# Kernel optimization log

Measured on AMD Instinct MI355X. Metric: run time of the kernel, lower is better.

The kernel has to match this reference:

```python
import jax, jax.numpy as jnp
import numpy as np
from jax import lax

B, N, NB = 1, 1600, 200
NOTE, ENC, ENCVEC = 128, 64, 16
OUT, MARGIN, TREG = 11, 32, 32
E = 12
FIN = NOTE + ENC + 2 * TREG + OUT + MARGIN   # 299 = net_params.final.input
SEC = OUT + MARGIN                           # 43 = GatedGraph secondary size
FBH = NOTE + ENC                             # final_beat_hidden_idx
SEQ_IT, G_IT = 2, 3
HEADS_M = 8


def setup_inputs():
    key = jax.random.key(0)
    ks = iter(jax.random.split(key, 64))
    nrm = lambda shape, s=0.05: jax.random.normal(next(ks), shape, jnp.float32) * s
    zeros = lambda shape: jnp.zeros(shape, jnp.float32)
    inp = {}
    inp["note_out"] = jax.random.normal(next(ks), (B, N, NOTE), jnp.float32)
    inp["perf_vec"] = jax.random.normal(next(ks), (B, ENCVEC), jnp.float32)
    inp["res_info"] = jax.random.normal(next(ks), (B, NB, 8), jnp.float32)
    # sparse musical-graph adjacency, one matrix per edge type
    inp["edges"] = (jax.random.uniform(next(ks), (E, N, N)) < 0.004).astype(jnp.float32)
    # sorted beat index per note, every beat non-empty (8 notes per beat)
    inp["beat_numbers"] = jnp.arange(N, dtype=jnp.int32) // (N // NB)
    inp["w_style"] = nrm((ENCVEC, ENC)); inp["b_style"] = zeros((ENC,))
    inp["w_init1"] = nrm((NOTE, ENC)); inp["b_init1"] = zeros((ENC,))
    inp["w_init2"] = nrm((ENC, OUT)); inp["b_init2"] = zeros((OUT,))
    inp["gg_wa"] = nrm((E, FIN, FIN)); inp["gg_ba"] = zeros((FIN,))
    inp["gg_wz"] = nrm((FIN, SEC)); inp["gg_wr"] = nrm((FIN, SEC)); inp["gg_wh"] = nrm((FIN, SEC))
    inp["gg_uz"] = nrm((SEC, SEC)); inp["gg_ur"] = nrm((SEC, SEC)); inp["gg_uh"] = nrm((SEC, SEC))
    inp["att_beat_w"] = nrm((OUT, OUT)); inp["att_beat_b"] = zeros((OUT,)); inp["att_beat_c"] = nrm((1, OUT), 1.0)
    inp["att_marg_w"] = nrm((MARGIN, MARGIN)); inp["att_marg_b"] = zeros((MARGIN,))
    inp["att_marg_c"] = nrm((HEADS_M, MARGIN // HEADS_M), 1.0)
    rnn_in = MARGIN + OUT + 8
    for l, din in ((0, rnn_in), (1, 2 * TREG)):
        for d in "fb":
            inp[f"lstm_wih_{l}{d}"] = nrm((4 * TREG, din))
            inp[f"lstm_whh_{l}{d}"] = nrm((4 * TREG, TREG))
            inp[f"lstm_b_{l}{d}"] = zeros((4 * TREG,))
    inp["w_tempo"] = nrm((2 * TREG, 1)); inp["b_tempo"] = zeros((1,))
    inp["w_fc1"] = nrm((FIN, MARGIN)); inp["b_fc1"] = zeros((MARGIN,))
    inp["w_fc2"] = nrm((MARGIN, OUT - 1)); inp["b_fc2"] = zeros((OUT - 1,))
    return inp


def _gated_graph(h, edges, wa, ba, wz, wr, wh, uz, ur, uh, iters):
    # h: (B,N,FIN), edges: (E,N,N). GGNN update on last SEC features.
    for _ in range(iters):
        agg = jnp.einsum('eij,bid->ebjd', edges, h)          # incoming msgs per edge type
        act = jnp.einsum('ebjd,eds->bjs', agg, wa) + ba      # (B,N,FIN)
        hs = h[..., -SEC:]
        z = jax.nn.sigmoid(act @ wz + hs @ uz)
        r = jax.nn.sigmoid(act @ wr + hs @ ur)
        cand = jnp.tanh(act @ wh + (r * hs) @ uh)
        hs = (1.0 - z) * hs + z * cand
        h = jnp.concatenate([h[..., :-SEC], hs], -1)
    return h


def _seg_attention(x, W, b, ctx, seg, num_seg):
    # ContextAttention pooled per beat segment (make_higher_node).
    Bb, T, D = x.shape
    H, hd = ctx.shape
    a = jnp.tanh(x @ W + b).reshape(Bb, T, H, hd)
    sim = jnp.einsum('bthd,hd->bth', a, ctx)
    def smax(s):  # segment softmax over notes within each beat, (T,H)
        m = jax.ops.segment_max(s, seg, num_segments=num_seg)
        e = jnp.exp(s - m[seg])
        zz = jax.ops.segment_sum(e, seg, num_segments=num_seg)
        return e / zz[seg]
    w = jax.vmap(smax)(sim)                                   # (B,T,H)
    xh = x.reshape(Bb, T, H, hd)
    pool = jax.vmap(lambda wi, xi: jax.ops.segment_sum(wi[:, :, None] * xi, seg, num_segments=num_seg))(w, xh)
    return pool.reshape(Bb, num_seg, D)


def _lstm_dir(x, wih, whh, b, reverse):
    Bb = x.shape[0]; H = whh.shape[1]
    def step(carry, xt):
        h, c = carry
        g = xt @ wih.T + h @ whh.T + b
        i, f, gg, o = jnp.split(g, 4, -1)
        c = jax.nn.sigmoid(f) * c + jax.nn.sigmoid(i) * jnp.tanh(gg)
        h = jax.nn.sigmoid(o) * jnp.tanh(c)
        return (h, c), h
    init = (jnp.zeros((Bb, H), x.dtype), jnp.zeros((Bb, H), x.dtype))
    _, hs = lax.scan(step, init, jnp.swapaxes(x, 0, 1), reverse=reverse)
    return jnp.swapaxes(hs, 0, 1)


def _bilstm(x, layers):
    for (wf, uf, bf, wb, ub, bb) in layers:
        x = jnp.concatenate([_lstm_dir(x, wf, uf, bf, False), _lstm_dir(x, wb, ub, bb, True)], -1)
    return x


def _forward(note_out, perf_vec, res_info, edges, beat_numbers,
             w_style, b_style, w_init1, b_init1, w_init2, b_init2,
             gg_wa, gg_ba, gg_wz, gg_wr, gg_wh, gg_uz, gg_ur, gg_uh,
             att_beat_w, att_beat_b, att_beat_c, att_marg_w, att_marg_b, att_marg_c,
             lstm_wih_0f, lstm_whh_0f, lstm_b_0f, lstm_wih_0b, lstm_whh_0b, lstm_b_0b,
             lstm_wih_1f, lstm_whh_1f, lstm_b_1f, lstm_wih_1b, lstm_whh_1b, lstm_b_1b,
             w_tempo, b_tempo, w_fc1, b_fc1, w_fc2, b_fc2):
    Bb, Nn, _ = note_out.shape
    # style_vector_expandor (dropout = identity in eval), broadcast to notes
    perf_z = jax.nn.relu(perf_vec @ w_style + b_style)
    perf_z = jnp.broadcast_to(perf_z[:, None, :], (Bb, Nn, ENC))
    init_out = jax.nn.relu(note_out @ w_init1 + b_init1) @ w_init2 + b_init2
    beat_hid0 = jnp.zeros((Bb, Nn, 2 * TREG), note_out.dtype)
    margin0 = jnp.zeros((Bb, Nn, MARGIN), note_out.dtype)
    out = jnp.concatenate([note_out, perf_z, beat_hid0, init_out, margin0], -1)  # (B,N,FIN)
    lstm_layers = [(lstm_wih_0f, lstm_whh_0f, lstm_b_0f, lstm_wih_0b, lstm_whh_0b, lstm_b_0b),
                   (lstm_wih_1f, lstm_whh_1f, lstm_b_1f, lstm_wih_1b, lstm_whh_1b, lstm_b_1b)]
    total = [init_out]
    final_out = init_out
    for _ in range(SEQ_IT):
        out = _gated_graph(out, edges, gg_wa, gg_ba, gg_wz, gg_wr, gg_wh, gg_uz, gg_ur, gg_uh, G_IT)
        init_o = out[..., -SEC:-MARGIN]          # (B,N,OUT)
        marg = out[..., -MARGIN:]                # (B,N,MARGIN)
        marg_beat = _seg_attention(marg, att_marg_w, att_marg_b, att_marg_c, beat_numbers, NB)
        out_beat = _seg_attention(init_o, att_beat_w, att_beat_b, att_beat_c, beat_numbers, NB)
        beat_cat = jnp.concatenate([out_beat, marg_beat, res_info], -1)  # (B,NB,51)
        rnn = _bilstm(beat_cat, lstm_layers)                             # (B,NB,64)
        tempo = rnn @ w_tempo + b_tempo                                  # (B,NB,1)
        tempos_sp = tempo[:, beat_numbers, :]    # span_beat_to_note_num
        rnn_sp = rnn[:, beat_numbers, :]
        out = jnp.concatenate([out[..., :FBH], rnn_sp, out[..., -SEC:]], -1)
        other = jax.nn.relu(out @ w_fc1 + b_fc1) @ w_fc2 + b_fc2         # (B,N,OUT-1)
        final_out = jnp.concatenate([tempos_sp, other], -1)              # (B,N,OUT)
        out = jnp.concatenate([out[..., :-SEC], final_out, out[..., -MARGIN:]], -1)
        total.append(final_out)
    return final_out, jnp.stack(total, 0)


def reference(note_out, perf_vec, res_info, edges, beat_numbers,
              w_style, b_style, w_init1, b_init1, w_init2, b_init2,
              gg_wa, gg_ba, gg_wz, gg_wr, gg_wh, gg_uz, gg_ur, gg_uh,
              att_beat_w, att_beat_b, att_beat_c, att_marg_w, att_marg_b, att_marg_c,
              lstm_wih_0f, lstm_whh_0f, lstm_b_0f, lstm_wih_0b, lstm_whh_0b, lstm_b_0b,
              lstm_wih_1f, lstm_whh_1f, lstm_b_1f, lstm_wih_1b, lstm_whh_1b, lstm_b_1b,
              w_tempo, b_tempo, w_fc1, b_fc1, w_fc2, b_fc2):
    return _forward(note_out, perf_vec, res_info, edges, beat_numbers,
                    w_style, b_style, w_init1, b_init1, w_init2, b_init2,
                    gg_wa, gg_ba, gg_wz, gg_wr, gg_wh, gg_uz, gg_ur, gg_uh,
                    att_beat_w, att_beat_b, att_beat_c, att_marg_w, att_marg_b, att_marg_c,
                    lstm_wih_0f, lstm_whh_0f, lstm_b_0f, lstm_wih_0b, lstm_whh_0b, lstm_b_0b,
                    lstm_wih_1f, lstm_whh_1f, lstm_b_1f, lstm_wih_1b, lstm_whh_1b, lstm_b_1b,
                    w_tempo, b_tempo, w_fc1, b_fc1, w_fc2, b_fc2)
```

## Files before the change

### kernel.cpp

```cpp
#include <hip/hip_runtime.h>
#include <stdint.h>

#define NN     1600
#define NBEAT  200
#define FINW   299
#define HSTR   300
#define SECW   43
#define EDG    12
#define C3     129
#define CM     128
#define DEG_CAP 256

#define NB_WA3   450
#define NB_INIT8 200
#define NB_SCAN  2560

#define K1C (-1.4426950408889634f)
#define K2C (-2.8853900817779268f)

#if __has_builtin(__builtin_amdgcn_exp2f)
__device__ __forceinline__ float fexp2(float x){ return __builtin_amdgcn_exp2f(x); }
#else
__device__ __forceinline__ float fexp2(float x){ return exp2f(x); }
#endif
#if __has_builtin(__builtin_amdgcn_rcpf)
__device__ __forceinline__ float frcp(float x){ return __builtin_amdgcn_rcpf(x); }
#else
__device__ __forceinline__ float frcp(float x){ return 1.0f/x; }
#endif

__device__ __forceinline__ float sigm(float x){ return frcp(1.f + fexp2(K1C*x)); }
__device__ __forceinline__ float tanh_(float x){ return __builtin_fmaf(frcp(1.f + fexp2(K2C*x)), 2.f, -1.f); }

__device__ __forceinline__ float gate_scale(int col){
  return (col >= 64 && col < 96) ? K2C : K1C;
}

__device__ __forceinline__ float swap_lo_to_hi(float v){
#if __has_builtin(__builtin_amdgcn_permlane32_swap)
  typedef unsigned u32x2 __attribute__((ext_vector_type(2)));
  u32x2 r = __builtin_amdgcn_permlane32_swap(__float_as_uint(v), __float_as_uint(v), false, false);
  return __uint_as_float(r[0]);
#else
  return __shfl(v, (int)(threadIdx.x & 31), 64);
#endif
}

constexpr size_t OFF_H    = 0;
constexpr size_t OFF_WA3  = OFF_H    + (size_t)NN*HSTR;
constexpr size_t OFF_WA3X = OFF_WA3  + (size_t)EDG*FINW*CM;
constexpr size_t OFF_B3   = OFF_WA3X + (size_t)EDG*FINW;
constexpr size_t OFF_MST  = OFF_B3   + 132;
constexpr size_t OFF_MSTX = OFF_MST  + (size_t)EDG*NN*CM;
constexpr size_t OFF_M3   = OFF_MSTX + (size_t)EDG*NN;
constexpr size_t OFF_M3X  = OFF_M3   + (size_t)EDG*NN*CM;
constexpr size_t OFF_CUR  = OFF_M3X  + (size_t)EDG*NN;
constexpr size_t OFF_ADJR = OFF_CUR  + NN;
constexpr size_t OFF_XW   = OFF_ADJR + (size_t)NN*DEG_CAP;
constexpr size_t OFF_RNN0 = OFF_XW   + (size_t)2*NBEAT*128;
constexpr size_t OFF_RNN1 = OFF_RNN0 + (size_t)NBEAT*64;

__global__ __launch_bounds__(192) void k_setup(
    const float* wa, const float* ba, const float* wz, const float* wr, const float* wh,
    const float* note, const float* pv, const float* w_style, const float* b_style,
    const float* w1, const float* b1, const float* w2, const float* b2,
    const float* edges, float* ws, float* dout){
  int blk = blockIdx.x;
  int t = threadIdx.x;
  __shared__ __align__(16) float smem[2392];
  if (blk < NB_WA3){
    float* lrow = smem;
    int base = blk*8;
    for (int x=t; x<8*299; x+=192){
      int r = x & 7, s = x >> 3;
      int R = base + r;
      float v = 0.f;
      if (R < 3588)       v = wa[(size_t)R*FINW + s];
      else if (R == 3588) v = ba[s];
      lrow[s*8 + r] = v;
    }
    __syncthreads();
    if (t < C3){
      const float* Wp; int cc;
      if (t<43){Wp=wz; cc=t;} else if (t<86){Wp=wr; cc=t-43;} else {Wp=wh; cc=t-86;}
      float acc[8];
      #pragma unroll
      for (int r=0;r<8;r++) acc[r]=0.f;
      for (int s=0;s<FINW;s++){
        float w = Wp[s*43+cc];
        float4 lo = *(const float4*)&lrow[s*8];
        float4 hi = *(const float4*)&lrow[s*8+4];
        acc[0]+=lo.x*w; acc[1]+=lo.y*w; acc[2]+=lo.z*w; acc[3]+=lo.w*w;
        acc[4]+=hi.x*w; acc[5]+=hi.y*w; acc[6]+=hi.z*w; acc[7]+=hi.w*w;
      }
      #pragma unroll
      for (int r=0;r<8;r++){
        int R = base + r;
        if (R < 3588){
          if (t<CM) ws[OFF_WA3 + (size_t)R*CM + t] = acc[r];
          else      ws[OFF_WA3X + R]               = acc[r];
        } else if (R == 3588){
          ws[OFF_B3 + t] = acc[r];
        }
      }
    }
  } else if (blk < NB_WA3 + NB_INIT8){
    float* ln    = smem;
    float* lh1   = smem + 1024;
    float* lo    = smem + 1536;
    float* lperf = smem + 1624;
    int i0 = (blk - NB_WA3)*8;
    for (int x=t; x<8*128; x+=192){
      int r = x >> 7, k = x & 127;
      ln[k*8 + r] = note[(size_t)(i0+r)*128 + k];
    }
    if (t>=64 && t<128){
      int u=t-64;
      float acc=b_style[u];
      for (int k=0;k<16;k++) acc += pv[k]*w_style[k*64+u];
      lperf[u]=fmaxf(acc,0.f);
    }
    __syncthreads();
    if (t<64){
      float acc[8];
      #pragma unroll
      for (int r=0;r<8;r++) acc[r]=b1[t];
      for (int k=0;k<128;k++){
        float w = w1[k*64+t];
        float4 a = *(const float4*)&ln[k*8];
        float4 b = *(const float4*)&ln[k*8+4];
        acc[0]+=a.x*w; acc[1]+=a.y*w; acc[2]+=a.z*w; acc[3]+=a.w*w;
        acc[4]+=b.x*w; acc[5]+=b.y*w; acc[6]+=b.z*w; acc[7]+=b.w*w;
      }
      #pragma unroll
      for (int r=0;r<8;r++) lh1[t*8+r]=fmaxf(acc[r],0.f);
    }
    __syncthreads();
    if (t<88){
      int r = t & 7, c = t >> 3;
      float acc=b2[c];
      for (int k=0;k<64;k++) acc += lh1[k*8+r]*w2[k*11+c];
      lo[r*11+c]=acc;
      dout[17600 + (size_t)(i0+r)*11 + c] = acc;
    }
    __syncthreads();
    #pragma unroll
    for (int r=0;r<8;r++){
      for (int c=t;c<FINW;c+=192){
        float v;
        if (c<128)      v=ln[c*8+r];
        else if (c<192) v=lperf[c-128];
        else if (c<256) v=0.f;
        else if (c<267) v=lo[r*11+(c-256)];
        else            v=0.f;
        ws[OFF_H + (size_t)(i0+r)*HSTR + c]=v;
      }
    }
  } else {
    int* cur  = (int*)(ws + OFF_CUR);
    int* adjr = (int*)(ws + OFF_ADJR);
    const uint4* p = (const uint4*)edges;
    const unsigned int nvec = 7680000u;
    const unsigned int stride = (unsigned int)NB_SCAN*192u;
    unsigned int v0 = (unsigned int)(blk - NB_WA3 - NB_INIT8)*192u + t;
    for (unsigned int b0 = v0; b0 < nvec; b0 += 4u*stride){
      unsigned int v1=b0+stride, v2=b0+2u*stride, v3=b0+3u*stride;
      bool g1=v1<nvec, g2=v2<nvec, g3=v3<nvec;
      uint4 w0 = p[b0];
      uint4 w1v = g1 ? p[v1] : make_uint4(0,0,0,0);
      uint4 w2v = g2 ? p[v2] : make_uint4(0,0,0,0);
      uint4 w3v = g3 ? p[v3] : make_uint4(0,0,0,0);
      uint4 wv[4] = {w0,w1v,w2v,w3v};
      unsigned int vv[4] = {b0,v1,v2,v3};
      #pragma unroll
      for (int u=0; u<4; u++){
        uint4 w = wv[u];
        if ((w.x|w.y|w.z|w.w)==0u) continue;
        unsigned int base = vv[u]*4u;
        unsigned int arr[4]={w.x,w.y,w.z,w.w};
        #pragma unroll
        for (int q=0;q<4;q++){
          if (arr[q]){
            unsigned int idx=base+q;
            unsigned int j=idx%1600u;
            int slot=atomicAdd(&cur[j],1);
            if (slot<DEG_CAP) adjr[j*DEG_CAP + slot]=(int)(idx/1600u);
          }
        }
      }
    }
  }
}

__global__ void k_mstat(float* ws, int dmain){
  int e = blockIdx.y; int i0 = blockIdx.x*8;
  int t = threadIdx.x;
  __shared__ float lh[8][256];
  __shared__ float lh2[8][44];
  const float* h = ws + OFF_H;
  for (int x=t; x<512; x+=64){
    int r = x>>6, dq = x&63;
    ((float4*)&lh[r][0])[dq] = ((const float4*)(h + (size_t)(i0+r)*HSTR))[dq];
  }
  for (int x=t; x<88; x+=64){
    int r = x/11, dq = x-r*11;
    ((float4*)&lh2[r][0])[dq] = ((const float4*)(h + (size_t)(i0+r)*HSTR + 256))[dq];
  }
  __syncthreads();
  const float* wm = ws + OFF_WA3 + (size_t)e*FINW*CM;
  int c0 = 2*t;
  float acc[8][2];
  #pragma unroll
  for (int r=0;r<8;r++){acc[r][0]=0.f;acc[r][1]=0.f;}
  for (int d=0; d<dmain; d+=4){
    float4 hv[8];
    #pragma unroll
    for (int r=0;r<8;r++) hv[r] = *(const float4*)&lh[r][d];
    #pragma unroll
    for (int dd=0;dd<4;dd++){
      float2 w = *(const float2*)(wm + (size_t)(d+dd)*CM + c0);
      #pragma unroll
      for (int r=0;r<8;r++){
        float hvv = ((const float*)&hv[r])[dd];
        acc[r][0] += hvv*w.x; acc[r][1] += hvv*w.y;
      }
    }
  }
  float* mst = ws + OFF_MST + ((size_t)e*NN + i0)*CM;
  #pragma unroll
  for (int r=0;r<8;r++) *(float2*)(mst + (size_t)r*CM + c0) = make_float2(acc[r][0],acc[r][1]);
  const float* wd = wm + (size_t)256*CM;
  for (int d=0; d<SECW; d++){
    float2 w = *(const float2*)(wd + (size_t)d*CM + c0);
    #pragma unroll
    for (int r=0;r<8;r++){
      float hvv = lh2[r][d];
      acc[r][0] += hvv*w.x; acc[r][1] += hvv*w.y;
    }
  }
  float* m3 = ws + OFF_M3 + ((size_t)e*NN + i0)*CM;
  #pragma unroll
  for (int r=0;r<8;r++) *(float2*)(m3 + (size_t)r*CM + c0) = make_float2(acc[r][0],acc[r][1]);
  if (t<8){
    const float* wx = ws + OFF_WA3X + (size_t)e*FINW;
    float a=0.f;
    for (int d=0; d<dmain; d++) a += lh[t][d]*wx[d];
    ws[OFF_MSTX + (size_t)e*NN + i0 + t] = a;
    for (int d=0; d<SECW; d++) a += lh2[t][d]*wx[256+d];
    ws[OFF_M3X + (size_t)e*NN + i0 + t] = a;
  }
}

__global__ void k_m3dyn(float* ws){
  int e=blockIdx.y, i0=blockIdx.x*8, t=threadIdx.x;
  __shared__ float lhs[8][44];
  const float* h = ws + OFF_H;
  for (int x=t; x<8*43; x+=64){ int r=x/43, d=x-r*43; lhs[r][d]=h[(size_t)(i0+r)*HSTR+256+d]; }
  __syncthreads();
  const float* wd  = ws + OFF_WA3 + ((size_t)e*FINW+256)*CM;
  const float* mst = ws + OFF_MST + ((size_t)e*NN+i0)*CM;
  int c0=2*t;
  float acc[8][2];
  #pragma unroll
  for (int r=0;r<8;r++){ float2 m=*(const float2*)(mst+(size_t)r*CM+c0); acc[r][0]=m.x; acc[r][1]=m.y; }
  for (int d=0; d<43; d++){
    float2 w=*(const float2*)(wd + (size_t)d*CM + c0);
    #pragma unroll
    for (int r=0;r<8;r++){ float hv=lhs[r][d]; acc[r][0]+=hv*w.x; acc[r][1]+=hv*w.y; }
  }
  float* m3 = ws + OFF_M3 + ((size_t)e*NN+i0)*CM;
  #pragma unroll
  for (int r=0;r<8;r++) *(float2*)(m3+(size_t)r*CM+c0)=make_float2(acc[r][0],acc[r][1]);
  if (t<8){
    float a = ws[OFF_MSTX + (size_t)e*NN+i0+t];
    const float* wx = ws + OFF_WA3X + (size_t)e*FINW + 256;
    for (int d=0;d<43;d++) a += lhs[t][d]*wx[d];
    ws[OFF_M3X + (size_t)e*NN+i0+t]=a;
  }
}

__global__ void k_agg_gru(float* ws, const float* uz, const float* ur, const float* uh){
  int j=blockIdx.x, t=threadIdx.x;
  __shared__ float lpre[C3];
  __shared__ float lhs[SECW];
  __shared__ float lrh[SECW];
  __shared__ int   ladj[DEG_CAP];
  float* h = ws + OFF_H;
  const int* cur =(const int*)(ws+OFF_CUR);
  const int* adjr=(const int*)(ws+OFF_ADJR) + (size_t)j*DEG_CAP;
  int cnt = cur[j]; if (cnt>DEG_CAP) cnt=DEG_CAP;
  for (int k=t;k<cnt;k+=128) ladj[k]=adjr[k];
  if (t<SECW) lhs[t] = h[(size_t)j*HSTR + 256 + t];
  __syncthreads();
  const float* M3=ws+OFF_M3; const float* M3X=ws+OFF_M3X;
  float a0 = ws[OFF_B3 + t];
  float ax = (t==0)? ws[OFF_B3+128] : 0.f;
  float p1=0.f,p2=0.f,p3=0.f,p4=0.f,p5=0.f,p6=0.f,p7=0.f;
  int k=0;
  for (; k+8<=cnt; k+=8){
    int r0=ladj[k],r1=ladj[k+1],r2=ladj[k+2],r3=ladj[k+3];
    int r4=ladj[k+4],r5=ladj[k+5],r6=ladj[k+6],r7=ladj[k+7];
    a0 += M3[(size_t)r0*CM+t];
    p1 += M3[(size_t)r1*CM+t];
    p2 += M3[(size_t)r2*CM+t];
    p3 += M3[(size_t)r3*CM+t];
    p4 += M3[(size_t)r4*CM+t];
    p5 += M3[(size_t)r5*CM+t];
    p6 += M3[(size_t)r6*CM+t];
    p7 += M3[(size_t)r7*CM+t];
    if (t==0) ax += ((M3X[r0]+M3X[r1])+(M3X[r2]+M3X[r3]))
                  + ((M3X[r4]+M3X[r5])+(M3X[r6]+M3X[r7]));
  }
  for (; k<cnt; k++){ int r=ladj[k]; a0+=M3[(size_t)r*CM+t]; if(t==0) ax+=M3X[r]; }
  a0 += ((p1+p2)+(p3+p4)) + ((p5+p6)+p7);
  lpre[t]=a0; if (t==0) lpre[128]=ax;
  __syncthreads();
  float z=0.f;
  if (t<SECW){
    float az=lpre[t], ar=lpre[43+t];
    for (int d=0;d<SECW;d++){ float hv=lhs[d]; az+=hv*uz[d*43+t]; ar+=hv*ur[d*43+t]; }
    z=sigm(az);
    float r=sigm(ar);
    lrh[t]=r*lhs[t];
  }
  __syncthreads();
  if (t<SECW){
    float ah=lpre[86+t];
    for (int d=0;d<SECW;d++) ah += lrh[d]*uh[d*43+t];
    float cand=tanh_(ah);
    h[(size_t)j*HSTR+256+t] = (1.f-z)*lhs[t] + z*cand;
  }
}

__global__ void k_attn_xw(float* ws, const float* mw, const float* mb, const float* mc,
                          const float* bw, const float* bb, const float* bc,
                          const float* res,
                          const float* w0f, const float* bia0f,
                          const float* w0b, const float* bia0b, float* xw){
  int b=blockIdx.x, t=threadIdx.x;
  float* h=ws+OFF_H;
  __shared__ float sm[8][8];
  __shared__ float wgt[8][8];
  __shared__ float sb[8];
  __shared__ float wb_[8];
  __shared__ float lb[52];
  int n=t>>3, hh=t&7;
  if (t<64){
    const float* mrow = h + (size_t)(b*8+n)*HSTR + 267;
    float sim=0.f;
    for (int d=0;d<4;d++){
      int c=hh*4+d;
      float acc=mb[c];
      for (int k=0;k<32;k++) acc += mrow[k]*mw[k*32+c];
      sim += tanh_(acc)*mc[c];
    }
    sm[n][hh]=sim;
  }
  if (t<8){
    const float* irow = h + (size_t)(b*8+t)*HSTR + 256;
    float sim=0.f;
    for (int d=0;d<11;d++){
      float acc=bb[d];
      for (int k=0;k<11;k++) acc += irow[k]*bw[k*11+d];
      sim += tanh_(acc)*bc[d];
    }
    sb[t]=sim;
  }
  __syncthreads();
  if (t<64){
    float m=-1e30f;
    for (int q=0;q<8;q++) m=fmaxf(m, sm[q][hh]);
    float Z=0.f;
    for (int q=0;q<8;q++) Z+=__expf(sm[q][hh]-m);
    wgt[n][hh]=__expf(sm[n][hh]-m)/Z;
  }
  if (t<8){
    float m=-1e30f;
    for (int q=0;q<8;q++) m=fmaxf(m, sb[q]);
    float Z=0.f;
    for (int q=0;q<8;q++) Z+=__expf(sb[q]-m);
    wb_[t]=__expf(sb[t]-m)/Z;
  }
  __syncthreads();
  if (t<32){
    int hh2=t>>2;
    float acc=0.f;
    for (int q=0;q<8;q++) acc += wgt[q][hh2]* h[(size_t)(b*8+q)*HSTR + 267 + t];
    lb[11+t]=acc;
  }
  if (t<11){
    float acc=0.f;
    for (int q=0;q<8;q++) acc += wb_[q]* h[(size_t)(b*8+q)*HSTR + 256 + t];
    lb[t]=acc;
  }
  if (t<8) lb[43+t]=res[b*8+t];
  __syncthreads();
  float acc0=bia0f[t], acc1=bia0b[t];
  for (int k=0;k<51;k++){
    float v=lb[k];
    acc0 += v*w0f[t*51+k];
    acc1 += v*w0b[t*51+k];
  }
  float sc = gate_scale(t);
  xw[((size_t)t)*NBEAT + b]       = acc0*sc;
  xw[((size_t)(128+t))*NBEAT + b] = acc1*sc;
}

__global__ void k_xw(const float* inp, int din, const float* wf, const float* bf_,
                     const float* wb, const float* bb_, float* xw){
  int bid=blockIdx.x; int tt=bid>>1, dir=bid&1;
  const float* w = dir? wb:wf; const float* bia = dir? bb_:bf_;
  __shared__ float rowl[64];
  int t=threadIdx.x;
  if (t<din) rowl[t]=inp[(size_t)tt*din+t];
  __syncthreads();
  float acc=bia[t];
  for (int k=0;k<din;k++) acc += rowl[k]*w[t*din+k];
  xw[((size_t)(dir*128 + t))*NBEAT + tt] = acc*gate_scale(t);
}

template<int DIR>
__device__ __forceinline__ void chunk8(int c, const float4& A0, const float4& A1,
    const float4& B0, const float4& B1,
    float* hu, float& creg, const float4* rA, const float4* rB,
    float cb1, float cb0, int l, float* out){
  float cxA[8] = {A0.x,A0.y,A0.z,A0.w,A1.x,A1.y,A1.z,A1.w};
  float cxB[8] = {B0.x,B0.y,B0.z,B0.w,B1.x,B1.y,B1.z,B1.w};
  float hst[8];
  #pragma unroll
  for (int u=0; u<8; u++){
    const int e = DIR ? (7-u) : u;
    float av[8], bv[8];
    #pragma unroll
    for (int q=0; q<8; q++){
      av[q] = hu[4*q+0]*rA[q].x + hu[4*q+1]*rA[q].y + hu[4*q+2]*rA[q].z + hu[4*q+3]*rA[q].w;
      bv[q] = hu[4*q+0]*rB[q].x + hu[4*q+1]*rB[q].y + hu[4*q+2]*rB[q].z + hu[4*q+3]*rB[q].w;
    }
    float accA = cxA[e] + (((av[0]+av[1])+(av[2]+av[3])) + ((av[4]+av[5])+(av[6]+av[7])));
    float accB = cxB[e] + (((bv[0]+bv[1])+(bv[2]+bv[3])) + ((bv[4]+bv[5])+(bv[6]+bv[7])));
    float pA  = frcp(1.f + fexp2(accA));
    float rBv = frcp(1.f + fexp2(accB));
    float pB  = __builtin_fmaf(rBv, cb1, cb0);
    float prod = pA * pB;
    float prodIn = swap_lo_to_hi(prod);
    creg = __builtin_fmaf(pA, creg, prodIn);
    float T = __builtin_fmaf(frcp(1.f + fexp2(creg)), 2.f, -1.f);
    float hnew = pB * T;
    hst[u] = hnew;
    #pragma unroll
    for (int d=0; d<32; d++)
      hu[d] = __uint_as_float(__builtin_amdgcn_readlane(__float_as_uint(hnew), 32+d));
  }
  if (l >= 32){
    int j = l - 32;
    #pragma unroll
    for (int u=0; u<8; u++){
      int s = c*8 + u;
      int tt = DIR ? (199 - s) : s;
      out[(size_t)tt*64 + DIR*32 + j] = hst[u];
    }
  }
}

template<int DIR>
__device__ __forceinline__ void lstm_scan(const float* xwT, const float* whh, float* out){
  const int l = threadIdx.x;
  const float sB = (l < 32) ? K2C : K1C;
  float4 rA[8], rB[8];
  #pragma unroll
  for (int q=0; q<8; q++){
    float4 a = *(const float4*)&whh[l*32 + q*4];
    float4 b = *(const float4*)&whh[(l+64)*32 + q*4];
    rA[q] = make_float4(a.x*K1C, a.y*K1C, a.z*K1C, a.w*K1C);
    rB[q] = make_float4(b.x*sB,  b.y*sB,  b.z*sB,  b.w*sB);
  }
  const float cb1 = (l < 32) ? (2.f*K2C) : 1.f;
  const float cb0 = (l < 32) ? (-K2C)    : 0.f;
  const float* xA = xwT + ((size_t)DIR*128 + l)*NBEAT;
  const float* xB = xwT + ((size_t)DIR*128 + 64 + l)*NBEAT;
  float hu[32];
  #pragma unroll
  for (int d=0; d<32; d++) hu[d] = 0.f;
  float creg = 0.f;
  float4 A0,A1,B0,B1, P0,P1,Q0,Q1;
#define LOADC(cidx, a0,a1,b0,b1) do {               \
    int _b = DIR ? (192 - (cidx)*8) : ((cidx)*8);   \
    a0 = *(const float4*)&xA[_b];                   \
    a1 = *(const float4*)&xA[_b+4];                 \
    b0 = *(const float4*)&xB[_b];                   \
    b1 = *(const float4*)&xB[_b+4];                 \
  } while(0)
  LOADC(0, A0,A1,B0,B1);
  for (int cc=0; cc<12; cc++){
    int c0 = 2*cc;
    LOADC(c0+1, P0,P1,Q0,Q1);
    chunk8<DIR>(c0,   A0,A1,B0,B1, hu, creg, rA, rB, cb1, cb0, l, out);
    LOADC(c0+2, A0,A1,B0,B1);
    chunk8<DIR>(c0+1, P0,P1,Q0,Q1, hu, creg, rA, rB, cb1, cb0, l, out);
  }
  chunk8<DIR>(24, A0,A1,B0,B1, hu, creg, rA, rB, cb1, cb0, l, out);
#undef LOADC
}

__global__ __launch_bounds__(64,1) void k_scan(const float* xwT, const float* whh_f,
                                               const float* whh_b, float* out){
  if (blockIdx.x == 0) lstm_scan<0>(xwT, whh_f, out);
  else                 lstm_scan<1>(xwT, whh_b, out);
}

__global__ void k_fc(float* ws, const int* bn, const float* w1, const float* b1,
                     const float* w2, const float* b2,
                     const float* wt, const float* bt, float* dout, int it){
  int i=blockIdx.x, t=threadIdx.x;
  __shared__ float row[FINW];
  __shared__ float hid[32];
  __shared__ float fo[11];
  float* h=ws+OFF_H;
  int b = bn[i];
  const float* rnn = ws+OFF_RNN1;
  for (int c=t;c<FINW;c+=64){
    float v;
    if (c>=192 && c<256){ v=rnn[(size_t)b*64 + c-192]; h[(size_t)i*HSTR+c]=v; }
    else v=h[(size_t)i*HSTR+c];
    row[c]=v;
  }
  float tv = rnn[(size_t)b*64 + t]*wt[t];
  #pragma unroll
  for (int off=32; off; off>>=1) tv += __shfl_xor(tv, off, 64);
  __syncthreads();
  if (t<32){
    float acc=b1[t];
    for (int k=0;k<FINW;k++) acc += row[k]*w1[k*32+t];
    hid[t]=fmaxf(acc,0.f);
  }
  __syncthreads();
  if (t<10){
    float acc=b2[t];
    for (int m=0;m<32;m++) acc += hid[m]*w2[m*10+t];
    fo[1+t]=acc;
  }
  if (t==0) fo[0]=tv + bt[0];
  __syncthreads();
  if (t<11){
    float v=fo[t];
    h[(size_t)i*HSTR+256+t]=v;
    dout[(size_t)(2+it)*17600 + i*11 + t]=v;
    if (it==1) dout[i*11+t]=v;
  }
}

extern "C" void kernel_launch(void* const* d_in, const int* in_sizes, int n_in,
                              void* d_out, int out_size, void* d_ws, size_t ws_size,
                              hipStream_t stream){
  (void)in_sizes; (void)n_in; (void)out_size; (void)ws_size;
  float* ws=(float*)d_ws;
  const float* note    =(const float*)d_in[0];
  const float* pv      =(const float*)d_in[1];
  const float* res     =(const float*)d_in[2];
  const float* edges   =(const float*)d_in[3];
  const int*   bn      =(const int*)d_in[4];
  const float* w_style =(const float*)d_in[5];
  const float* b_style =(const float*)d_in[6];
  const float* w_init1 =(const float*)d_in[7];
  const float* b_init1 =(const float*)d_in[8];
  const float* w_init2 =(const float*)d_in[9];
  const float* b_init2 =(const float*)d_in[10];
  const float* gg_wa   =(const float*)d_in[11];
  const float* gg_ba   =(const float*)d_in[12];
  const float* gg_wz   =(const float*)d_in[13];
  const float* gg_wr   =(const float*)d_in[14];
  const float* gg_wh   =(const float*)d_in[15];
  const float* gg_uz   =(const float*)d_in[16];
  const float* gg_ur   =(const float*)d_in[17];
  const float* gg_uh   =(const float*)d_in[18];
  const float* abw     =(const float*)d_in[19];
  const float* abb     =(const float*)d_in[20];
  const float* abc     =(const float*)d_in[21];
  const float* amw     =(const float*)d_in[22];
  const float* amb     =(const float*)d_in[23];
  const float* amc     =(const float*)d_in[24];
  const float* wih0f   =(const float*)d_in[25];
  const float* whh0f   =(const float*)d_in[26];
  const float* b0f     =(const float*)d_in[27];
  const float* wih0b   =(const float*)d_in[28];
  const float* whh0b   =(const float*)d_in[29];
  const float* b0b     =(const float*)d_in[30];
  const float* wih1f   =(const float*)d_in[31];
  const float* whh1f   =(const float*)d_in[32];
  const float* b1f     =(const float*)d_in[33];
  const float* wih1b   =(const float*)d_in[34];
  const float* whh1b   =(const float*)d_in[35];
  const float* b1b     =(const float*)d_in[36];
  const float* w_tempo =(const float*)d_in[37];
  const float* b_tempo =(const float*)d_in[38];
  const float* w_fc1   =(const float*)d_in[39];
  const float* b_fc1   =(const float*)d_in[40];
  const float* w_fc2   =(const float*)d_in[41];
  const float* b_fc2   =(const float*)d_in[42];
  float* dout=(float*)d_out;

  hipMemsetAsync(ws+OFF_CUR, 0, NN*sizeof(int), stream);
  k_setup<<<NB_WA3+NB_INIT8+NB_SCAN,192,0,stream>>>(
      gg_wa,gg_ba,gg_wz,gg_wr,gg_wh,
      note,pv,w_style,b_style,w_init1,b_init1,w_init2,b_init2,
      edges,ws,dout);

  for (int it=0; it<2; it++){
    k_mstat<<<dim3(200,12),64,0,stream>>>(ws, it==0 ? 192 : 256);
    k_agg_gru<<<NN,128,0,stream>>>(ws,gg_uz,gg_ur,gg_uh);
    for (int g=1; g<3; g++){
      k_m3dyn<<<dim3(200,12),64,0,stream>>>(ws);
      k_agg_gru<<<NN,128,0,stream>>>(ws,gg_uz,gg_ur,gg_uh);
    }
    k_attn_xw<<<NBEAT,128,0,stream>>>(ws,amw,amb,amc,abw,abb,abc,res,
                                      wih0f,b0f,wih0b,b0b,ws+OFF_XW);
    k_scan<<<2,64,0,stream>>>(ws+OFF_XW,whh0f,whh0b,ws+OFF_RNN0);
    k_xw<<<2*NBEAT,128,0,stream>>>(ws+OFF_RNN0,64,wih1f,b1f,wih1b,b1b,ws+OFF_XW);
    k_scan<<<2,64,0,stream>>>(ws+OFF_XW,whh1f,whh1b,ws+OFF_RNN1);
    k_fc<<<NN,64,0,stream>>>(ws,bn,w_fc1,b_fc1,w_fc2,b_fc2,w_tempo,b_tempo,dout,it);
  }
}
```

Measured before the change: 741.6 us.

## Fuse GRU propagation steps into one cooperative kernel with grid barriers

Replaces the five separate aggregate-GRU and message-update launches per iteration with one cooperative persistent kernel of 1024 blocks. The phases are separated by a software grid barrier built on atomic counters. This removes kernel launch gaps and tail effects between small dependent kernels. In exchange it adds atomic barrier spin cost, relies on all blocks being co-resident, and falls back to separate launches if the cooperative launch fails.

```diff
diff --git a/kernel.cpp b/kernel.cpp
--- a/kernel.cpp
+++ b/kernel.cpp
@@ -14,6 +14,8 @@
 #define NB_WA3   450
 #define NB_INIT8 200
 #define NB_SCAN  2560
+
+#define GRUB 1024
 
 #define K1C (-1.4426950408889634f)
 #define K2C (-2.8853900817779268f)
@@ -55,10 +57,30 @@
 constexpr size_t OFF_M3   = OFF_MSTX + (size_t)EDG*NN;
 constexpr size_t OFF_M3X  = OFF_M3   + (size_t)EDG*NN*CM;
 constexpr size_t OFF_CUR  = OFF_M3X  + (size_t)EDG*NN;
-constexpr size_t OFF_ADJR = OFF_CUR  + NN;
+constexpr size_t OFF_BAR  = OFF_CUR  + NN;
+constexpr size_t OFF_ADJR = OFF_BAR  + 4;
 constexpr size_t OFF_XW   = OFF_ADJR + (size_t)NN*DEG_CAP;
 constexpr size_t OFF_RNN0 = OFF_XW   + (size_t)2*NBEAT*128;
 constexpr size_t OFF_RNN1 = OFF_RNN0 + (size_t)NBEAT*64;
+
+__device__ __forceinline__ void grid_barrier(int* bar, int* gen, int nblk){
+  __syncthreads();
+  if (threadIdx.x == 0){
+    __threadfence();
+    int g = __hip_atomic_load(gen, __ATOMIC_RELAXED, __HIP_MEMORY_SCOPE_AGENT);
+    int a = __hip_atomic_fetch_add(bar, 1, __ATOMIC_ACQ_REL, __HIP_MEMORY_SCOPE_AGENT);
+    if (a == nblk-1){
+      __hip_atomic_store(bar, 0,   __ATOMIC_RELAXED, __HIP_MEMORY_SCOPE_AGENT);
+      __hip_atomic_store(gen, g+1, __ATOMIC_RELEASE, __HIP_MEMORY_SCOPE_AGENT);
+    } else {
+      while (__hip_atomic_load(gen, __ATOMIC_RELAXED, __HIP_MEMORY_SCOPE_AGENT) == g){
+        __builtin_amdgcn_s_sleep(2);
+      }
+    }
+    __threadfence();
+  }
+  __syncthreads();
+}
 
 __global__ __launch_bounds__(192) void k_setup(
     const float* wa, const float* ba, const float* wz, const float* wr, const float* wh,
@@ -251,40 +273,13 @@
   }
 }
 
-__global__ void k_m3dyn(float* ws){
-  int e=blockIdx.y, i0=blockIdx.x*8, t=threadIdx.x;
-  __shared__ float lhs[8][44];
-  const float* h = ws + OFF_H;
-  for (int x=t; x<8*43; x+=64){ int r=x/43, d=x-r*43; lhs[r][d]=h[(size_t)(i0+r)*HSTR+256+d]; }
-  __syncthreads();
-  const float* wd  = ws + OFF_WA3 + ((size_t)e*FINW+256)*CM;
-  const float* mst = ws + OFF_MST + ((size_t)e*NN+i0)*CM;
-  int c0=2*t;
-  float acc[8][2];
-  #pragma unroll
-  for (int r=0;r<8;r++){ float2 m=*(const float2*)(mst+(size_t)r*CM+c0); acc[r][0]=m.x; acc[r][1]=m.y; }
-  for (int d=0; d<43; d++){
-    float2 w=*(const float2*)(wd + (size_t)d*CM + c0);
-    #pragma unroll
-    for (int r=0;r<8;r++){ float hv=lhs[r][d]; acc[r][0]+=hv*w.x; acc[r][1]+=hv*w.y; }
-  }
-  float* m3 = ws + OFF_M3 + ((size_t)e*NN+i0)*CM;
-  #pragma unroll
-  for (int r=0;r<8;r++) *(float2*)(m3+(size_t)r*CM+c0)=make_float2(acc[r][0],acc[r][1]);
-  if (t<8){
-    float a = ws[OFF_MSTX + (size_t)e*NN+i0+t];
-    const float* wx = ws + OFF_WA3X + (size_t)e*FINW + 256;
-    for (int d=0;d<43;d++) a += lhs[t][d]*wx[d];
-    ws[OFF_M3X + (size_t)e*NN+i0+t]=a;
-  }
-}
-
-__global__ void k_agg_gru(float* ws, const float* uz, const float* ur, const float* uh){
-  int j=blockIdx.x, t=threadIdx.x;
-  __shared__ float lpre[C3];
-  __shared__ float lhs[SECW];
-  __shared__ float lrh[SECW];
-  __shared__ int   ladj[DEG_CAP];
+__device__ __forceinline__ void agg_gru_body(float* ws, const float* uz, const float* ur,
+                                             const float* uh, float* sm, int j){
+  int t = threadIdx.x;
+  float* lpre = sm;
+  float* lhs  = sm + 132;
+  float* lrh  = sm + 176;
+  int*   ladj = (int*)(sm + 224);
   float* h = ws + OFF_H;
   const int* cur =(const int*)(ws+OFF_CUR);
   const int* adjr=(const int*)(ws+OFF_ADJR) + (size_t)j*DEG_CAP;
@@ -330,6 +325,67 @@
     float cand=tanh_(ah);
     h[(size_t)j*HSTR+256+t] = (1.f-z)*lhs[t] + z*cand;
   }
+}
+
+__device__ __forceinline__ void m3dyn_body(float* ws, float* sm, int u){
+  int e = u % EDG, i0 = (u / EDG) * 8;
+  int t = threadIdx.x & 63;
+  float* lhs = sm + (threadIdx.x >> 6) * 352;
+  const float* h = ws + OFF_H;
+  for (int x=t; x<8*43; x+=64){ int r=x/43, d=x-r*43; lhs[r*44+d]=h[(size_t)(i0+r)*HSTR+256+d]; }
+  __syncthreads();
+  const float* wd  = ws + OFF_WA3 + ((size_t)e*FINW+256)*CM;
+  const float* mst = ws + OFF_MST + ((size_t)e*NN+i0)*CM;
+  int c0=2*t;
+  float acc[8][2];
+  #pragma unroll
+  for (int r=0;r<8;r++){ float2 m=*(const float2*)(mst+(size_t)r*CM+c0); acc[r][0]=m.x; acc[r][1]=m.y; }
+  for (int d=0; d<43; d++){
+    float2 w=*(const float2*)(wd + (size_t)d*CM + c0);
+    #pragma unroll
+    for (int r=0;r<8;r++){ float hv=lhs[r*44+d]; acc[r][0]+=hv*w.x; acc[r][1]+=hv*w.y; }
+  }
+  float* m3 = ws + OFF_M3 + ((size_t)e*NN+i0)*CM;
+  #pragma unroll
+  for (int r=0;r<8;r++) *(float2*)(m3+(size_t)r*CM+c0)=make_float2(acc[r][0],acc[r][1]);
+  if (t<8){
+    float a = ws[OFF_MSTX + (size_t)e*NN+i0+t];
+    const float* wx = ws + OFF_WA3X + (size_t)e*FINW + 256;
+    for (int d=0;d<43;d++) a += lhs[t*44+d]*wx[d];
+    ws[OFF_M3X + (size_t)e*NN+i0+t]=a;
+  }
+}
+
+__global__ __launch_bounds__(128) void k_gru6(float* ws, const float* uz, const float* ur,
+                                              const float* uh){
+  int* bar = (int*)(ws + OFF_BAR);
+  int* gen = bar + 1;
+  __shared__ __align__(16) float sm[704];
+  #pragma unroll 1
+  for (int ph=0; ph<3; ph++){
+    for (int j = blockIdx.x; j < NN; j += GRUB){
+      agg_gru_body(ws, uz, ur, uh, sm, j);
+      __syncthreads();
+    }
+    if (ph < 2){
+      grid_barrier(bar, gen, GRUB);
+      for (int u = blockIdx.x*2 + (int)(threadIdx.x>>6); u < EDG*NBEAT; u += 2*GRUB){
+        m3dyn_body(ws, sm, u);
+        __syncthreads();
+      }
+      grid_barrier(bar, gen, GRUB);
+    }
+  }
+}
+
+__global__ __launch_bounds__(128) void k_agg_gru_sep(float* ws, const float* uz,
+                                                     const float* ur, const float* uh){
+  __shared__ __align__(16) float sm[704];
+  agg_gru_body(ws, uz, ur, uh, sm, blockIdx.x);
+}
+__global__ __launch_bounds__(128) void k_m3dyn_sep(float* ws){
+  __shared__ __align__(16) float sm[704];
+  m3dyn_body(ws, sm, blockIdx.x*2 + (int)(threadIdx.x>>6));
 }
 
 __global__ void k_attn_xw(float* ws, const float* mw, const float* mb, const float* mc,
@@ -599,7 +655,7 @@
   const float* b_fc2   =(const float*)d_in[42];
   float* dout=(float*)d_out;
 
-  hipMemsetAsync(ws+OFF_CUR, 0, NN*sizeof(int), stream);
+  hipMemsetAsync(ws+OFF_CUR, 0, (NN+4)*sizeof(int), stream);
   k_setup<<<NB_WA3+NB_INIT8+NB_SCAN,192,0,stream>>>(
       gg_wa,gg_ba,gg_wz,gg_wr,gg_wh,
       note,pv,w_style,b_style,w_init1,b_init1,w_init2,b_init2,
@@ -607,10 +663,17 @@
 
   for (int it=0; it<2; it++){
     k_mstat<<<dim3(200,12),64,0,stream>>>(ws, it==0 ? 192 : 256);
-    k_agg_gru<<<NN,128,0,stream>>>(ws,gg_uz,gg_ur,gg_uh);
-    for (int g=1; g<3; g++){
-      k_m3dyn<<<dim3(200,12),64,0,stream>>>(ws);
-      k_agg_gru<<<NN,128,0,stream>>>(ws,gg_uz,gg_ur,gg_uh);
+    {
+      void* cargs[4] = { (void*)&ws, (void*)&gg_uz, (void*)&gg_ur, (void*)&gg_uh };
+      hipError_t ce = hipLaunchCooperativeKernel((const void*)k_gru6, dim3(GRUB),
+                                                 dim3(128), cargs, 0, stream);
+      if (ce != hipSuccess){
+        k_agg_gru_sep<<<NN,128,0,stream>>>(ws,gg_uz,gg_ur,gg_uh);
+        for (int g=1; g<3; g++){
+          k_m3dyn_sep<<<EDG*NBEAT/2,128,0,stream>>>(ws);
+          k_agg_gru_sep<<<NN,128,0,stream>>>(ws,gg_uz,gg_ur,gg_uh);
+        }
+      }
     }
     k_attn_xw<<<NBEAT,128,0,stream>>>(ws,amw,amb,amc,abw,abb,abc,res,
                                       wih0f,b0f,wih0b,b0b,ws+OFF_XW);
```

After: 2.117 ms. 2.85x slower.

## Fuse both LSTM layer scans and layer-1 input projection into one kernel

Applied to the files above, without the earlier changes.

Replaces the layer-0 scan, the layer-1 input-projection kernel and the layer-1 scan with a single one-block, 512-thread kernel. Two waves run the forward and backward scans, and all threads compute the layer-1 input projection between `__syncthreads` barriers. This removes two kernel launches and their inter-kernel gaps per outer iteration. In exchange, the 400-row projection, formerly spread over 400 blocks, now runs on a single CU, which may lengthen that phase.

```diff
diff --git a/kernel.cpp b/kernel.cpp
--- a/kernel.cpp
+++ b/kernel.cpp
@@ -406,19 +406,6 @@
   xw[((size_t)(128+t))*NBEAT + b] = acc1*sc;
 }
 
-__global__ void k_xw(const float* inp, int din, const float* wf, const float* bf_,
-                     const float* wb, const float* bb_, float* xw){
-  int bid=blockIdx.x; int tt=bid>>1, dir=bid&1;
-  const float* w = dir? wb:wf; const float* bia = dir? bb_:bf_;
-  __shared__ float rowl[64];
-  int t=threadIdx.x;
-  if (t<din) rowl[t]=inp[(size_t)tt*din+t];
-  __syncthreads();
-  float acc=bia[t];
-  for (int k=0;k<din;k++) acc += rowl[k]*w[t*din+k];
-  xw[((size_t)(dir*128 + t))*NBEAT + tt] = acc*gate_scale(t);
-}
-
 template<int DIR>
 __device__ __forceinline__ void chunk8(int c, const float4& A0, const float4& A1,
     const float4& B0, const float4& B1,
@@ -463,8 +450,7 @@
 }
 
 template<int DIR>
-__device__ __forceinline__ void lstm_scan(const float* xwT, const float* whh, float* out){
-  const int l = threadIdx.x;
+__device__ __forceinline__ void lstm_scan(int l, const float* xwT, const float* whh, float* out){
   const float sB = (l < 32) ? K2C : K1C;
   float4 rA[8], rB[8];
   #pragma unroll
@@ -502,10 +488,35 @@
 #undef LOADC
 }
 
-__global__ __launch_bounds__(64,1) void k_scan(const float* xwT, const float* whh_f,
-                                               const float* whh_b, float* out){
-  if (blockIdx.x == 0) lstm_scan<0>(xwT, whh_f, out);
-  else                 lstm_scan<1>(xwT, whh_b, out);
+__global__ __launch_bounds__(512,1) void k_beat(float* ws,
+    const float* whh0f, const float* whh0b,
+    const float* wih1f, const float* b1f, const float* wih1b, const float* b1b,
+    const float* whh1f, const float* whh1b){
+  const int tid = threadIdx.x;
+  float* xw0  = ws + OFF_XW;
+  float* rnn0 = ws + OFF_RNN0;
+  float* rnn1 = ws + OFF_RNN1;
+  if (tid < 64)        lstm_scan<0>(tid,      xw0, whh0f, rnn0);
+  else if (tid < 128)  lstm_scan<1>(tid & 63, xw0, whh0b, rnn0);
+  __syncthreads();
+  {
+    int sub = tid >> 7;
+    int c   = tid & 127;
+    float scl = gate_scale(c);
+    for (int u = sub; u < 2*NBEAT; u += 4){
+      int tt = u >> 1, dir = u & 1;
+      const float* w   = dir ? wih1b : wih1f;
+      const float* bia = dir ? b1b   : b1f;
+      const float* row = rnn0 + (size_t)tt*64;
+      float acc = bia[c];
+      #pragma unroll 8
+      for (int k=0; k<64; k++) acc += row[k]*w[c*64+k];
+      xw0[((size_t)(dir*128 + c))*NBEAT + tt] = acc*scl;
+    }
+  }
+  __syncthreads();
+  if (tid < 64)        lstm_scan<0>(tid,      xw0, whh1f, rnn1);
+  else if (tid < 128)  lstm_scan<1>(tid & 63, xw0, whh1b, rnn1);
 }
 
 __global__ void k_fc(float* ws, const int* bn, const float* w1, const float* b1,
@@ -614,9 +625,7 @@
     }
     k_attn_xw<<<NBEAT,128,0,stream>>>(ws,amw,amb,amc,abw,abb,abc,res,
                                       wih0f,b0f,wih0b,b0b,ws+OFF_XW);
-    k_scan<<<2,64,0,stream>>>(ws+OFF_XW,whh0f,whh0b,ws+OFF_RNN0);
-    k_xw<<<2*NBEAT,128,0,stream>>>(ws+OFF_RNN0,64,wih1f,b1f,wih1b,b1b,ws+OFF_XW);
-    k_scan<<<2,64,0,stream>>>(ws+OFF_XW,whh1f,whh1b,ws+OFF_RNN1);
+    k_beat<<<1,512,0,stream>>>(ws,whh0f,whh0b,wih1f,b1f,wih1b,b1b,whh1f,whh1b);
     k_fc<<<NN,64,0,stream>>>(ws,bn,w_fc1,b_fc1,w_fc2,b_fc2,w_tempo,b_tempo,dout,it);
   }
 }
```

After: 1.732 ms. 2.34x slower.
